# Kernel optimization log

Measured on AMD Instinct MI355X. Metric: run time of the kernel, lower is better.

## Reference

```python
import jax, jax.numpy as jnp
import numpy as np

DIM = 1024; VOCAB = 32000; HEADS = 16; HEAD_DIM = DIM // HEADS
SEG = 128; NPT = 16; WIDTH = 128
THETA = 0.1; ETA = 0.9; ALPHA = 0.01; EPS = 1e-6  # neural-memory lr / momentum / weight-decay


def l2n(x):
    return x / (jnp.linalg.norm(x, axis=-1, keepdims=True) + EPS)


def mlp(p, x):
    # 2-layer memory MLP: dim -> width -> dim, SiLU
    W1, b1, W2, b2 = p
    return jax.nn.silu(x @ W1 + b1) @ W2 + b2


def setup_inputs() -> dict:
    key = jax.random.key(0)
    ks = jax.random.split(key, 12)
    g = lambda k, s: jax.random.normal(k, s, jnp.float32) * 0.02
    z = lambda n: jnp.zeros((n,), jnp.float32)
    return {
        "x": jax.random.randint(ks[0], (2, 512), 0, VOCAB),
        "embedding": g(ks[1], (VOCAB, DIM)),
        "persistent": g(ks[2], (NPT, DIM)),
        "Wq": g(ks[3], (DIM, DIM)), "bq": z(DIM),
        "Wk": g(ks[4], (DIM, DIM)), "bk": z(DIM),
        "Wv": g(ks[5], (DIM, DIM)), "bv": z(DIM),
        "attn_in_w": g(ks[6], (DIM, 3 * DIM)), "attn_in_b": z(3 * DIM),
        "attn_out_w": g(ks[7], (DIM, DIM)), "attn_out_b": z(DIM),
        "mW1": g(ks[8], (DIM, WIDTH)), "mb1": z(WIDTH),
        "mW2": g(ks[9], (WIDTH, DIM)), "mb2": z(DIM),
        "head_w": g(ks[10], (DIM, VOCAB)), "head_b": z(VOCAB),
    }


def reference(x, embedding, persistent, Wq, bq, Wk, bk, Wv, bv,
              attn_in_w, attn_in_b, attn_out_w, attn_out_b,
              mW1, mb1, mW2, mb2, head_w, head_b):
    B, N = x.shape
    x_emb = embedding[x]  # [B, N, D]
    pad = (-N) % SEG
    if pad:
        x_emb = jnp.pad(x_emb, ((0, 0), (0, pad), (0, 0)))
    S = x_emb.shape[1] // SEG
    segs = x_emb.reshape(B, S, SEG, DIM).transpose(1, 0, 2, 3)  # [S, B, L, D]

    T = NPT + 2 * SEG  # persistent + retrieved memory + segment tokens
    causal = jnp.triu(jnp.ones((T, T), bool), 1)

    def mha(xc):  # [B, T, D] -> [B, T, D], torch nn.MultiheadAttention math
        q, k, v = jnp.split(xc @ attn_in_w + attn_in_b, 3, axis=-1)
        split = lambda t: t.reshape(B, T, HEADS, HEAD_DIM).transpose(0, 2, 1, 3)
        q, k, v = split(q), split(k), split(v)
        scores = jnp.einsum('bhqd,bhkd->bhqk', q, k) / np.sqrt(HEAD_DIM).astype(np.float32)
        scores = jnp.where(causal, -jnp.inf, scores)
        out = jnp.einsum('bhqk,bhkd->bhqd', jax.nn.softmax(scores, axis=-1), v)
        return out.transpose(0, 2, 1, 3).reshape(B, T, DIM) @ attn_out_w + attn_out_b

    # per-sample memory params (leading B axis) + zero momentum
    params0 = tuple(jnp.broadcast_to(w, (B,) + w.shape) for w in (mW1, mb1, mW2, mb2))
    mom0 = tuple(jnp.zeros_like(p) for p in params0)

    def mem_loss(p, k, v):
        e = mlp(p, k) - v
        return jnp.sum(e * e)

    def tok_step(carry, tok):  # tok: [B, D] -- one test-time gradient step on memory
        p, m = carry
        k = jax.lax.stop_gradient(l2n(tok @ Wk + bk))  # stop_grad_k=True
        v = tok @ Wv + bv                               # stop_grad_v=False
        grads = jax.vmap(jax.grad(mem_loss))(p, k, v)
        m = jax.tree.map(lambda mm, g: ETA * mm - THETA * g, m, grads)
        p = jax.tree.map(lambda pp, mm: (1.0 - ALPHA) * pp + mm, p, m)
        return (p, m), None

    retrieve = jax.vmap(mlp)  # vmap over per-sample memory params

    def seg_step(carry, segment):  # segment: [B, L, D]
        p, m = carry
        h = retrieve(p, l2n(segment @ Wq + bq))
        combined = jnp.concatenate(
            [jnp.broadcast_to(persistent, (B, NPT, DIM)), h, segment], axis=1)
        seg_out = mha(combined)[:, -SEG:, :]
        (p, m), _ = jax.lax.scan(tok_step, (p, m), seg_out.transpose(1, 0, 2))
        mem_out = retrieve(p, l2n(seg_out @ Wq + bq))
        return (p, m), seg_out * mem_out

    _, outs = jax.lax.scan(seg_step, (params0, mom0), segs)  # outs: [S, B, L, D]
    full = outs.transpose(1, 0, 2, 3).reshape(B, S * SEG, DIM)[:, :N, :]
    return full @ head_w + head_b
```

## Files before the change

kernel.cpp:

```cpp
#include <hip/hip_runtime.h>
#include <math.h>

#define D_    1024
#define B_    2
#define N_    512
#define SEG_  128
#define NSEG_ 4
#define NPT_  16
#define T_    272
#define NH_   16
#define HD_   64
#define W_    128
#define V_    32000

#define THETA_ 0.1f
#define ETA_   0.9f
#define PDEC_  0.99f
#define EPSN_  1e-6f
#define NBLK_ 16
#define FSTR_ 32

typedef __bf16 bf16x8 __attribute__((ext_vector_type(8)));
typedef float  f32x4  __attribute__((ext_vector_type(4)));

static const size_t XEMB = 0;
static const size_t OUTS = XEMB + (size_t)B_*N_*D_;
static const size_t PW1  = OUTS + (size_t)B_*N_*D_;
static const size_t PB1  = PW1  + (size_t)B_*D_*W_;
static const size_t PW2T = PB1  + (size_t)B_*W_;
static const size_t PB2  = PW2T + (size_t)B_*D_*W_;
static const size_t MOM  = PB2  + (size_t)B_*D_;
static const size_t MW1  = MOM;
static const size_t MB1  = MW1  + (size_t)B_*D_*W_;
static const size_t MW2T = MB1  + (size_t)B_*W_;
static const size_t MB2  = MW2T + (size_t)B_*D_*W_;
static const size_t MOMSZ = (size_t)B_*(D_*W_ + W_ + D_*W_ + D_);
static const size_t Q1   = MOM  + MOMSZ;
static const size_t AH   = Q1   + (size_t)B_*SEG_*D_;
static const size_t HBUF = AH   + (size_t)B_*SEG_*W_;
static const size_t COMB = HBUF + (size_t)B_*SEG_*D_;
static const size_t QKV  = COMB + (size_t)B_*T_*D_;
static const size_t ATTN = QKV  + (size_t)B_*T_*3*D_;
static const size_t SEGO = ATTN + (size_t)B_*SEG_*D_;
static const size_t KM   = SEGO + (size_t)B_*SEG_*D_;
static const size_t VM   = KM   + (size_t)B_*SEG_*D_;
static const size_t MEMO = VM   + (size_t)B_*SEG_*D_;
static const size_t WSEND = MEMO + (size_t)B_*SEG_*D_;

static const size_t AQ1K  = QKV;
static const size_t AQ1KM = AQ1K  + 32768;
static const size_t AGRAM = AQ1KM + 32768;
static const size_t ADZ1  = AGRAM + 32768;
static const size_t AA1H  = ADZ1  + 32768;
static const size_t AEH   = AA1H  + 32768;
static const size_t AEXA1 = AEH + (size_t)B_*SEG_*D_;
static const size_t AEXSP = AEXA1 + 512;
static const size_t AEXR  = AEXSP + 8192;
static const size_t AEXEE = AEXR  + 8192;
static const size_t COEF  = WSEND;
static const size_t ZEROB = COEF + 512;
static const size_t CBAR  = ZEROB + 128;

__device__ __forceinline__ float sigf(float x) { return 1.f/(1.f+expf(-x)); }

__device__ __forceinline__ void gstore(float* p, float v) {
  __hip_atomic_store(p, v, __ATOMIC_RELAXED, __HIP_MEMORY_SCOPE_AGENT);
}
__device__ __forceinline__ float gload(const float* p) {
  return __hip_atomic_load(p, __ATOMIC_RELAXED, __HIP_MEMORY_SCOPE_AGENT);
}

__device__ __forceinline__ void bsplit(float a, short& h, short& l) {
  unsigned u = __builtin_bit_cast(unsigned, a);
  unsigned hb = (u + 0x7fffu + ((u >> 16) & 1u)) >> 16;
  h = (short)hb;
  float hf = __builtin_bit_cast(float, hb << 16);
  float r = a - hf;
  unsigned ur = __builtin_bit_cast(unsigned, r);
  unsigned lb = (ur + 0x7fffu + ((ur >> 16) & 1u)) >> 16;
  l = (short)lb;
}

template<int BT, int SILU>
__global__ __launch_bounds__(256) void k_gemm(
    const float* __restrict__ A, const float* __restrict__ Bm,
    const float* __restrict__ bias, float* __restrict__ C,
    int M, int N, int K, long sA, long sB, long sC, long sBias)
{
  __shared__ float As[16][68];
  __shared__ float Bs[16][68];
  int bz = blockIdx.z;
  A += bz*sA; Bm += bz*sB; C += bz*sC; bias += bz*sBias;
  int n0 = blockIdx.x*64, m0 = blockIdx.y*64;
  int tid = threadIdx.x;
  int tx = tid & 15, ty = tid >> 4;
  int r  = tid >> 2;
  int kq = (tid & 3) * 4;
  float acc[4][4] = {};
  for (int k0 = 0; k0 < K; k0 += 16) {
    {
      int row = m0 + r;
      float4 v = make_float4(0.f,0.f,0.f,0.f);
      if (row < M) v = *(const float4*)(A + (long)row*K + k0 + kq);
      As[kq+0][r]=v.x; As[kq+1][r]=v.y; As[kq+2][r]=v.z; As[kq+3][r]=v.w;
    }
    if (BT) {
      int row = n0 + r;
      float4 v = *(const float4*)(Bm + (long)row*K + k0 + kq);
      Bs[kq+0][r]=v.x; Bs[kq+1][r]=v.y; Bs[kq+2][r]=v.z; Bs[kq+3][r]=v.w;
    } else {
      int c = tid & 63, r4 = tid >> 6;
      #pragma unroll
      for (int p = 0; p < 4; p++) {
        int kk = r4 + p*4;
        Bs[kk][c] = Bm[(long)(k0+kk)*N + n0 + c];
      }
    }
    __syncthreads();
    #pragma unroll
    for (int kk = 0; kk < 16; kk++) {
      float av[4], bv[4];
      #pragma unroll
      for (int i=0;i<4;i++) av[i] = As[kk][ty*4+i];
      #pragma unroll
      for (int j=0;j<4;j++) bv[j] = Bs[kk][tx*4+j];
      #pragma unroll
      for (int i=0;i<4;i++)
        #pragma unroll
        for (int j=0;j<4;j++)
          acc[i][j] = fmaf(av[i], bv[j], acc[i][j]);
    }
    __syncthreads();
  }
  #pragma unroll
  for (int i=0;i<4;i++) {
    int row = m0 + ty*4 + i;
    if (row >= M) continue;
    #pragma unroll
    for (int j=0;j<4;j++) {
      int col = n0 + tx*4 + j;
      float v = acc[i][j] + bias[col];
      if (SILU) v = v * sigf(v);
      C[(long)row*N + col] = v;
    }
  }
}

__global__ __launch_bounds__(256) void k_gemm2(
    const float* __restrict__ A, const float* __restrict__ B1,
    const float* __restrict__ B2, float* __restrict__ C1, float* __restrict__ C2,
    int K, long sA, long sB, long sC)
{
  __shared__ float As[16][68];
  __shared__ float B1s[16][68];
  __shared__ float B2s[16][68];
  int bz = blockIdx.z;
  A += bz*sA; B1 += bz*sB; B2 += bz*sB; C1 += bz*sC; C2 += bz*sC;
  int n0 = blockIdx.x*64, m0 = blockIdx.y*64;
  int tid = threadIdx.x;
  int tx = tid & 15, ty = tid >> 4;
  int r  = tid >> 2;
  int kq = (tid & 3) * 4;
  float acc1[4][4] = {}, acc2[4][4] = {};
  for (int k0 = 0; k0 < K; k0 += 16) {
    {
      float4 v = *(const float4*)(A + (long)(m0+r)*K + k0 + kq);
      As[kq+0][r]=v.x; As[kq+1][r]=v.y; As[kq+2][r]=v.z; As[kq+3][r]=v.w;
    }
    {
      int c = tid & 63, r4 = tid >> 6;
      #pragma unroll
      for (int p = 0; p < 4; p++) {
        int kk = r4 + p*4;
        B1s[kk][c] = B1[(long)(k0+kk)*W_ + n0 + c];
        B2s[kk][c] = B2[(long)(k0+kk)*W_ + n0 + c];
      }
    }
    __syncthreads();
    #pragma unroll
    for (int kk = 0; kk < 16; kk++) {
      float av[4], b1v[4], b2v[4];
      #pragma unroll
      for (int i=0;i<4;i++) av[i] = As[kk][ty*4+i];
      #pragma unroll
      for (int j=0;j<4;j++) { b1v[j] = B1s[kk][tx*4+j]; b2v[j] = B2s[kk][tx*4+j]; }
      #pragma unroll
      for (int i=0;i<4;i++)
        #pragma unroll
        for (int j=0;j<4;j++) {
          acc1[i][j] = fmaf(av[i], b1v[j], acc1[i][j]);
          acc2[i][j] = fmaf(av[i], b2v[j], acc2[i][j]);
        }
    }
    __syncthreads();
  }
  #pragma unroll
  for (int i=0;i<4;i++) {
    int row = m0 + ty*4 + i;
    #pragma unroll
    for (int j=0;j<4;j++) {
      int col = n0 + tx*4 + j;
      C1[(long)row*W_ + col] = acc1[i][j];
      C2[(long)row*W_ + col] = acc2[i][j];
    }
  }
}

__global__ __launch_bounds__(256) void k_gemm128(
    const float* __restrict__ A, const float* __restrict__ Bm,
    const float* __restrict__ bias, float* __restrict__ C,
    int M, int N, int K)
{
  __shared__ float As[16][132];
  __shared__ float Bs[16][132];
  int n0 = blockIdx.x*128, m0 = blockIdx.y*128;
  int tid = threadIdx.x;
  int tx = tid & 15, ty = tid >> 4;
  int ar = tid >> 1, ak = (tid & 1) * 8;
  int bk = tid >> 4, bn = (tid & 15) * 8;
  int arow = min(m0 + ar, M-1);
  float acc[8][8] = {};
  for (int k0 = 0; k0 < K; k0 += 16) {
    {
      const float* ap = A + (long)arow*K + k0 + ak;
      float4 v0 = *(const float4*)(ap);
      float4 v1 = *(const float4*)(ap+4);
      As[ak+0][ar]=v0.x; As[ak+1][ar]=v0.y; As[ak+2][ar]=v0.z; As[ak+3][ar]=v0.w;
      As[ak+4][ar]=v1.x; As[ak+5][ar]=v1.y; As[ak+6][ar]=v1.z; As[ak+7][ar]=v1.w;
      const float* bp = Bm + (long)(k0+bk)*N + n0 + bn;
      *(float4*)(&Bs[bk][bn])   = *(const float4*)(bp);
      *(float4*)(&Bs[bk][bn+4]) = *(const float4*)(bp+4);
    }
    __syncthreads();
    #pragma unroll
    for (int kk = 0; kk < 16; kk++) {
      float av[8], bv[8];
      #pragma unroll
      for (int i=0;i<8;i++) av[i] = As[kk][ty*8+i];
      #pragma unroll
      for (int j=0;j<8;j++) bv[j] = Bs[kk][tx*8+j];
      #pragma unroll
      for (int i=0;i<8;i++)
        #pragma unroll
        for (int j=0;j<8;j++)
          acc[i][j] = fmaf(av[i], bv[j], acc[i][j]);
    }
    __syncthreads();
  }
  #pragma unroll
  for (int i=0;i<8;i++) {
    int row = m0 + ty*8 + i;
    if (row >= M) continue;
    #pragma unroll
    for (int j=0;j<8;j++) acc[i][j] += bias[n0 + tx*8 + j];
    *(float4*)(C + (long)row*N + n0 + tx*8)     = make_float4(acc[i][0],acc[i][1],acc[i][2],acc[i][3]);
    *(float4*)(C + (long)row*N + n0 + tx*8 + 4) = make_float4(acc[i][4],acc[i][5],acc[i][6],acc[i][7]);
  }
}

__global__ __launch_bounds__(256) void k_head_mfma(
    const float* __restrict__ A, const float* __restrict__ Bm,
    const float* __restrict__ bias, float* __restrict__ C,
    int M, int N, int K)
{
  __shared__ short Ah[128][48];
  __shared__ short Al[128][48];
  __shared__ short Bh[32][132];
  __shared__ short Bl[32][132];
  int n0 = blockIdx.x*128, m0 = blockIdx.y*128;
  int tid = threadIdx.x;
  int wave = tid >> 6, lane = tid & 63;
  int wm = (wave >> 1) * 64, wn = (wave & 1) * 64;
  int lrow = lane & 15, lk = (lane >> 4) * 8;
  f32x4 acc[4][4] = {};
  for (int k0 = 0; k0 < K; k0 += 32) {
    __syncthreads();
    {
      int r = tid >> 1, kq = (tid & 1) * 16;
      const float* ap = A + (long)(m0 + r)*K + k0 + kq;
      #pragma unroll
      for (int q = 0; q < 16; q += 4) {
        float4 v = *(const float4*)(ap + q);
        short h0,l0,h1,l1,h2,l2,h3,l3;
        bsplit(v.x,h0,l0); bsplit(v.y,h1,l1); bsplit(v.z,h2,l2); bsplit(v.w,h3,l3);
        short4 hh = make_short4(h0,h1,h2,h3), ll = make_short4(l0,l1,l2,l3);
        *(short4*)&Ah[r][kq+q] = hh;
        *(short4*)&Al[r][kq+q] = ll;
      }
    }
    {
      int kr = tid >> 3, nq = (tid & 7) * 16;
      const float* bp = Bm + (long)(k0 + kr)*N + n0 + nq;
      #pragma unroll
      for (int q = 0; q < 16; q += 4) {
        float4 v = *(const float4*)(bp + q);
        short h0,l0,h1,l1,h2,l2,h3,l3;
        bsplit(v.x,h0,l0); bsplit(v.y,h1,l1); bsplit(v.z,h2,l2); bsplit(v.w,h3,l3);
        *(short4*)&Bh[kr][nq+q] = make_short4(h0,h1,h2,h3);
        *(short4*)&Bl[kr][nq+q] = make_short4(l0,l1,l2,l3);
      }
    }
    __syncthreads();
    bf16x8 bh[4], bl[4];
    #pragma unroll
    for (int nf = 0; nf < 4; nf++) {
      int col = wn + nf*16 + lrow;
      #pragma unroll
      for (int j = 0; j < 8; j++) {
        bh[nf][j] = __builtin_bit_cast(__bf16, Bh[lk+j][col]);
        bl[nf][j] = __builtin_bit_cast(__bf16, Bl[lk+j][col]);
      }
    }
    #pragma unroll
    for (int mf = 0; mf < 4; mf++) {
      int arow2 = wm + mf*16 + lrow;
      bf16x8 ah = *(const bf16x8*)&Ah[arow2][lk];
      bf16x8 al = *(const bf16x8*)&Al[arow2][lk];
      #pragma unroll
      for (int nf = 0; nf < 4; nf++) {
        acc[mf][nf] = __builtin_amdgcn_mfma_f32_16x16x32_bf16(ah, bh[nf], acc[mf][nf], 0, 0, 0);
        acc[mf][nf] = __builtin_amdgcn_mfma_f32_16x16x32_bf16(ah, bl[nf], acc[mf][nf], 0, 0, 0);
        acc[mf][nf] = __builtin_amdgcn_mfma_f32_16x16x32_bf16(al, bh[nf], acc[mf][nf], 0, 0, 0);
      }
    }
  }
  #pragma unroll
  for (int mf = 0; mf < 4; mf++) {
    #pragma unroll
    for (int nf = 0; nf < 4; nf++) {
      int col = n0 + wn + nf*16 + lrow;
      float bv = bias[col];
      #pragma unroll
      for (int j = 0; j < 4; j++) {
        int row = m0 + wm + mf*16 + (lane >> 4)*4 + j;
        C[(long)row*N + col] = acc[mf][nf][j] + bv;
      }
    }
  }
}

__global__ void k_embed(const int* __restrict__ x, const float* __restrict__ emb,
                        float* __restrict__ xe)
{
  int row = blockIdx.x, tid = threadIdx.x;
  int idx = x[row];
  float4 v = *(const float4*)(emb + (long)idx*D_ + tid*4);
  *(float4*)(xe + (long)row*D_ + tid*4) = v;
}

#define PER_ 263296L
__global__ void k_init(const float* __restrict__ mW1in, const float* __restrict__ mb1in,
                       const float* __restrict__ mW2in, const float* __restrict__ mb2in,
                       float* __restrict__ pW1, float* __restrict__ pb1,
                       float* __restrict__ pW2T, float* __restrict__ pb2)
{
  long g = (long)blockIdx.x*256 + threadIdx.x;
  if (g >= 2*PER_) return;
  int b = (int)(g / PER_);
  long rr = g % PER_;
  if (rr < 131072)       pW1[(long)b*131072 + rr] = mW1in[rr];
  else if (rr < 131200)  pb1[b*W_ + (rr-131072)] = mb1in[rr-131072];
  else if (rr < 262272) { long l = rr-131200; int j=(int)(l>>7), h=(int)(l&127);
                          pW2T[(long)b*131072 + l] = mW2in[(long)h*D_ + j]; }
  else                   pb2[b*D_ + (rr-262272)] = mb2in[rr-262272];
}

__global__ void k_coef(float* __restrict__ c)
{
  if (blockIdx.x == 0 && threadIdx.x == 0) {
    c[0] = 1.f; c[128] = 1.f;
    float A = 1.f, eta_d = 1.f;
    for (int d = 1; d < 128; d++) {
      eta_d *= ETA_;
      A = PDEC_*A + eta_d;
      c[d] = A;
      c[128 + d] = eta_d;
    }
    c[256] = 1.f;
    float bp = 1.f;
    for (int t = 1; t <= 128; t++) { bp *= PDEC_; c[256 + t] = bp; }
  }
}

__global__ __launch_bounds__(256) void k_l2n(float* __restrict__ X)
{
  long row = blockIdx.x;
  float* p = X + row*D_;
  int tid = threadIdx.x;
  float4 v = *(float4*)(p + tid*4);
  float ss = v.x*v.x + v.y*v.y + v.z*v.z + v.w*v.w;
  for (int o=32;o;o>>=1) ss += __shfl_xor(ss,o);
  __shared__ float wsum[4];
  if ((tid&63)==0) wsum[tid>>6] = ss;
  __syncthreads();
  float tot = wsum[0]+wsum[1]+wsum[2]+wsum[3];
  float sc = 1.f/(sqrtf(tot)+EPSN_);
  v.x*=sc; v.y*=sc; v.z*=sc; v.w*=sc;
  *(float4*)(p + tid*4) = v;
}

__global__ void k_concat(const float* __restrict__ pers, const float* __restrict__ h,
                         const float* __restrict__ xemb, int s, float* __restrict__ comb)
{
  int row = blockIdx.x, b = blockIdx.y, tid = threadIdx.x;
  const float* src;
  if (row < NPT_)            src = pers + (long)row*D_;
  else if (row < NPT_+SEG_)  src = h    + ((long)b*SEG_ + (row-NPT_))*D_;
  else                       src = xemb + ((long)b*N_ + s*SEG_ + (row-NPT_-SEG_))*D_;
  float4 v = *(const float4*)(src + tid*4);
  *(float4*)(comb + ((long)b*T_ + row)*D_ + tid*4) = v;
}

__global__ __launch_bounds__(256) void k_attn(const float* __restrict__ qkv,
                                              float* __restrict__ outp)
{
  __shared__ float sQ[16][68];
  __shared__ float sKV[64][68];
  __shared__ float sS[16][273];
  int qt = blockIdx.x, head = blockIdx.y, b = blockIdx.z;
  int tid = threadIdx.x;
  const float* base = qkv + (long)b*T_*3*D_;
  int qoff = head*HD_, koff = D_ + head*HD_, voff = 2*D_ + head*HD_;
  int qrow0 = NPT_ + SEG_ + qt*16;
  {
    int rr = tid>>4, c4 = (tid&15)*4;
    float4 v = *(const float4*)(base + (long)(qrow0+rr)*3*D_ + qoff + c4);
    sQ[rr][c4]=v.x; sQ[rr][c4+1]=v.y; sQ[rr][c4+2]=v.z; sQ[rr][c4+3]=v.w;
  }
  __syncthreads();
  for (int j0 = 0; j0 < T_; j0 += 64) {
    int chunk = min(64, T_ - j0);
    {
      int jj = tid>>2, cq = (tid&3)*16;
      if (jj < chunk) {
        #pragma unroll
        for (int q4=0;q4<4;q4++) {
          float4 v = *(const float4*)(base + (long)(j0+jj)*3*D_ + koff + cq + q4*4);
          sKV[jj][cq+q4*4]=v.x; sKV[jj][cq+q4*4+1]=v.y; sKV[jj][cq+q4*4+2]=v.z; sKV[jj][cq+q4*4+3]=v.w;
        }
      }
    }
    __syncthreads();
    int rr = tid>>4, jj0 = tid&15;
    #pragma unroll
    for (int p=0;p<4;p++) {
      int jj = jj0 + p*16;
      if (jj < chunk) {
        float s = 0.f;
        #pragma unroll 8
        for (int c=0;c<HD_;c++) s = fmaf(sQ[rr][c], sKV[jj][c], s);
        s *= 0.125f;
        int jg = j0 + jj, qg = qrow0 + rr;
        if (jg > qg) s = -3.0e38f;
        sS[rr][jg] = s;
      }
    }
    __syncthreads();
  }
  {
    int rr = tid>>4, l16 = tid&15;
    float m = -3.4e38f;
    for (int j=l16; j<T_; j+=16) m = fmaxf(m, sS[rr][j]);
    for (int o=8;o;o>>=1) m = fmaxf(m, __shfl_xor(m,o));
    float sum = 0.f;
    for (int j=l16; j<T_; j+=16) { float e = expf(sS[rr][j]-m); sS[rr][j] = e; sum += e; }
    for (int o=8;o;o>>=1) sum += __shfl_xor(sum,o);
    float inv = 1.f/sum;
    for (int j=l16; j<T_; j+=16) sS[rr][j] *= inv;
  }
  __syncthreads();
  float acc[4] = {0.f,0.f,0.f,0.f};
  int rr = tid>>4, c4 = (tid&15)*4;
  for (int j0 = 0; j0 < T_; j0 += 64) {
    int chunk = min(64, T_ - j0);
    {
      int jj = tid>>2, cq = (tid&3)*16;
      if (jj < chunk) {
        #pragma unroll
        for (int q4=0;q4<4;q4++) {
          float4 v = *(const float4*)(base + (long)(j0+jj)*3*D_ + voff + cq + q4*4);
          sKV[jj][cq+q4*4]=v.x; sKV[jj][cq+q4*4+1]=v.y; sKV[jj][cq+q4*4+2]=v.z; sKV[jj][cq+q4*4+3]=v.w;
        }
      }
    }
    __syncthreads();
    for (int jj=0; jj<chunk; jj++) {
      float p = sS[rr][j0+jj];
      #pragma unroll
      for (int i=0;i<4;i++) acc[i] = fmaf(p, sKV[jj][c4+i], acc[i]);
    }
    __syncthreads();
  }
  float4 o4 = make_float4(acc[0],acc[1],acc[2],acc[3]);
  *(float4*)(outp + ((long)(b*SEG_) + qt*16 + rr)*D_ + head*HD_ + c4) = o4;
}

__device__ __forceinline__ void gbar(int* flags, int blk, int gen)
{
  asm volatile("s_waitcnt vmcnt(0) lgkmcnt(0)" ::: "memory");
  __syncthreads();
  if (threadIdx.x == 0)
    __hip_atomic_store(flags + blk*FSTR_, gen, __ATOMIC_RELAXED, __HIP_MEMORY_SCOPE_AGENT);
  if (threadIdx.x < NBLK_) {
    while (__hip_atomic_load(flags + threadIdx.x*FSTR_, __ATOMIC_RELAXED,
                             __HIP_MEMORY_SCOPE_AGENT) < gen)
      __builtin_amdgcn_s_sleep(1);
  }
  __syncthreads();
}

__global__ __launch_bounds__(256) void k_scan(
  const float* __restrict__ pW2T, const float* __restrict__ mW2T,
  float* __restrict__ pb1, float* __restrict__ mb1,
  float* __restrict__ pb2, float* __restrict__ mb2,
  const float* __restrict__ Vm,
  const float* __restrict__ q1k, const float* __restrict__ q1km,
  const float* __restrict__ G,
  float* __restrict__ dz1o, float* __restrict__ a1o, float* __restrict__ eo,
  float* __restrict__ exA1, float* __restrict__ exSP,
  float* __restrict__ exR, float* __restrict__ exEE,
  const float* __restrict__ coef, int* __restrict__ barbase, int seg)
{
  __shared__ float sW[64][132];
  __shared__ float sMW[64][132];
  __shared__ float sEh[128][66];
  __shared__ float sA1h[128][9];
  __shared__ float sDZ[128][9];
  __shared__ float sQ1K[128][8];
  __shared__ float sQ1KM[128][8];
  __shared__ float sAt[128];
  __shared__ float sBp[129];
  __shared__ float sB1[8], sMB1[8], sZ1[8], sR[8];
  __shared__ float sB2[64], sMB2[64], sE[64];
  __shared__ float sA1t[128];
  __shared__ float sS[128];
  __shared__ float sEEc[128];

  int b = blockIdx.y, blk = blockIdx.x, tid = threadIdx.x;
  int j0 = blk*64, h0 = blk*8;
  int* flags = barbase + b*(NBLK_*FSTR_);
  int gbase = seg*1000;

  for (int i = tid; i < 64*128; i += 256) {
    int jj = i >> 7, h = i & 127;
    sW[jj][h]  = pW2T[(long)b*131072 + (long)(j0+jj)*128 + h];
    sMW[jj][h] = mW2T[(long)b*131072 + (long)(j0+jj)*128 + h];
  }
  for (int i = tid; i < 128*8; i += 256) {
    int t2 = i >> 3, hh = i & 7;
    sQ1K[t2][hh]  = q1k [((long)b*SEG_ + t2)*W_ + h0 + hh];
    sQ1KM[t2][hh] = q1km[((long)b*SEG_ + t2)*W_ + h0 + hh];
  }
  if (tid < 128) sAt[tid] = coef[tid];
  for (int i = tid; i < 129; i += 256) sBp[i] = coef[256 + i];
  if (tid < 8)  { sB1[tid] = pb1[b*W_ + h0 + tid]; sMB1[tid] = mb1[b*W_ + h0 + tid]; }
  if (tid >= 64 && tid < 128) {
    int jj = tid - 64;
    sB2[jj] = pb2[b*D_ + j0 + jj]; sMB2[jj] = mb2[b*D_ + j0 + jj];
  }
  __syncthreads();

  for (int t = 0; t < SEG_; ++t) {
    int par = t & 1;
    float bp = sBp[t];
    float ca = (t > 0) ? ETA_*sAt[t-1] : 0.f;

    if (t > 0 && tid < 8) {
      float mm = ETA_*sMB1[tid] - THETA_*sDZ[t-1][tid];
      sMB1[tid] = mm; sB1[tid] = PDEC_*sB1[tid] + mm;
    }
    __syncthreads();
    {
      int hh = tid >> 5, lane = tid & 31;
      float acc = 0.f;
      const float* Grow = G + ((long)b*SEG_ + t)*SEG_;
      for (int u = lane; u < t; u += 32)
        acc += sAt[t-1-u] * Grow[u] * sDZ[u][hh];
      for (int o = 16; o; o >>= 1) acc += __shfl_xor(acc, o);
      if (lane == 0) {
        int h = h0 + hh;
        float z1 = bp*sQ1K[t][hh] + ca*sQ1KM[t][hh] + sB1[hh] - THETA_*acc;
        sZ1[hh] = z1;
        float a1 = z1 * sigf(z1);
        sA1h[t][hh] = a1;
        gstore(&exA1[(long)par*(B_*W_) + b*W_ + h], a1);
      }
    }
    __syncthreads();
    if (tid < t) {
      float acc = 0.f;
      #pragma unroll
      for (int hh2 = 0; hh2 < 8; hh2++) acc += sA1h[tid][hh2]*sA1h[t][hh2];
      gstore(&exSP[(((long)par*B_ + b)*NBLK_ + blk)*W_ + tid], acc);
    }
    gbar(flags, blk, gbase + t*2 + 1);

    float rA1 = 0.f, rSP = 0.f;
    if (tid < 128) {
      rA1 = gload(&exA1[(long)par*(B_*W_) + b*W_ + tid]);
    } else {
      int u = tid - 128;
      if (u < t) {
        #pragma unroll
        for (int k2 = 0; k2 < NBLK_; k2++)
          rSP += gload(&exSP[(((long)par*B_ + b)*NBLK_ + k2)*W_ + u]);
      }
    }
    if (t > 0 && tid < 64) {
      float mm = ETA_*sMB2[tid] - 2.f*THETA_*sEh[t-1][tid];
      sMB2[tid] = mm; sB2[tid] = PDEC_*sB2[tid] + mm;
    }
    if (tid < 128) {
      sA1t[tid] = rA1;
    } else {
      int u = tid - 128;
      if (u < t) sS[u] = -2.f*THETA_*sAt[t-1-u]*rSP;
    }
    __syncthreads();
    {
      int jj = tid >> 2, l4 = tid & 3;
      float g0 = 0.f, gm = 0.f;
      for (int h = l4; h < 128; h += 4) {
        g0 = fmaf(sW[jj][h],  sA1t[h], g0);
        gm = fmaf(sMW[jj][h], sA1t[h], gm);
      }
      float corr = 0.f;
      for (int u = l4; u < t; u += 4) corr = fmaf(sS[u], sEh[u][jj], corr);
      float tot = bp*g0 + ca*gm + corr;
      tot += __shfl_xor(tot, 1); tot += __shfl_xor(tot, 2);
      if (l4 == 0) {
        float e = tot + sB2[jj] - Vm[((long)b*SEG_ + t)*D_ + j0 + jj];
        sEh[t][jj] = e; sE[jj] = e;
      }
    }
    __syncthreads();
    {
      int h = tid >> 1, l = tid & 1;
      float r0 = 0.f, rm = 0.f;
      for (int jj = l*32; jj < l*32+32; jj++) {
        r0 = fmaf(sW[jj][h],  sE[jj], r0);
        rm = fmaf(sMW[jj][h], sE[jj], rm);
      }
      float rc = bp*r0 + ca*rm;
      rc += __shfl_xor(rc, 1);
      if (l == 0) gstore(&exR[(((long)par*B_ + b)*NBLK_ + blk)*W_ + h], rc);
    }
    {
      int u = tid >> 1, l = tid & 1;
      if (u < t) {
        float acc = 0.f;
        for (int jj = l*32; jj < l*32+32; jj++) acc = fmaf(sEh[u][jj], sE[jj], acc);
        acc += __shfl_xor(acc, 1);
        if (l == 0) gstore(&exEE[(((long)par*B_ + b)*NBLK_ + blk)*W_ + u], acc);
      }
    }
    gbar(flags, blk, gbase + t*2 + 2);

    if (tid < t) {
      float s = 0.f;
      #pragma unroll
      for (int k2 = 0; k2 < NBLK_; k2++)
        s += gload(&exEE[(((long)par*B_ + b)*NBLK_ + k2)*W_ + tid]);
      sEEc[tid] = -2.f*THETA_*sAt[t-1-tid]*s;
    }
    if (tid >= 128 && tid < 136) {
      int hh = tid - 128;
      float s = 0.f;
      #pragma unroll
      for (int k2 = 0; k2 < NBLK_; k2++)
        s += gload(&exR[(((long)par*B_ + b)*NBLK_ + k2)*W_ + h0 + hh]);
      sR[hh] = s;
    }
    __syncthreads();
    {
      int hh = tid >> 5, lane = tid & 31;
      float acc = 0.f;
      for (int u = lane; u < t; u += 32) acc = fmaf(sEEc[u], sA1h[u][hh], acc);
      for (int o = 16; o; o >>= 1) acc += __shfl_xor(acc, o);
      if (lane == 0) {
        float z = sZ1[hh];
        float sg = sigf(z);
        float dz = 2.f*(sR[hh] + acc) * sg*(1.f + z*(1.f - sg));
        sDZ[t][hh] = dz;
      }
    }
    __syncthreads();
  }

  for (int i = tid; i < 128*8; i += 256) {
    int t2 = i >> 3, hh = i & 7;
    dz1o[((long)b*SEG_ + t2)*W_ + h0 + hh] = sDZ[t2][hh];
    a1o [((long)b*SEG_ + t2)*W_ + h0 + hh] = sA1h[t2][hh];
  }
  for (int i = tid; i < 128*64; i += 256) {
    int t2 = i >> 6, jj = i & 63;
    eo[((long)b*SEG_ + t2)*D_ + j0 + jj] = sEh[t2][jj];
  }
  if (tid < 8) {
    float mm = ETA_*sMB1[tid] - THETA_*sDZ[127][tid];
    mb1[b*W_ + h0 + tid] = mm;
    pb1[b*W_ + h0 + tid] = PDEC_*sB1[tid] + mm;
  } else if (tid >= 64 && tid < 128) {
    int jj = tid - 64;
    float mm = ETA_*sMB2[jj] - 2.f*THETA_*sEh[127][jj];
    mb2[b*D_ + j0 + jj] = mm;
    pb2[b*D_ + j0 + jj] = PDEC_*sB2[jj] + mm;
  }
}

__global__ __launch_bounds__(256) void k_recon(
  float* __restrict__ pW1, float* __restrict__ mW1,
  float* __restrict__ pW2T, float* __restrict__ mW2T,
  const float* __restrict__ KMp, const float* __restrict__ Eh,
  const float* __restrict__ DZ1, const float* __restrict__ A1h,
  const float* __restrict__ coef)
{
  __shared__ float s1[16][33];
  __shared__ float s2[16][65];
  __shared__ float sCA[128], sCE[128];
  int dt = blockIdx.x, ht = blockIdx.y, kb = blockIdx.z;
  int kind = kb >> 1, b = kb & 1;
  int tid = threadIdx.x;
  int d0 = dt*32, hb = ht*64;
  const float* in1 = (kind ? Eh : KMp) + (long)b*SEG_*D_;
  const float* in2 = (kind ? A1h : DZ1) + (long)b*SEG_*W_;
  float* Pb = (kind ? pW2T : pW1) + (long)b*131072;
  float* Mb = (kind ? mW2T : mW1) + (long)b*131072;
  float f = kind ? -2.f*THETA_ : -THETA_;
  if (tid < 128) {
    sCA[tid] = f*coef[127 - tid];
    sCE[tid] = f*coef[128 + 127 - tid];
  }
  __syncthreads();
  int dd = tid >> 3, le = tid & 7;
  float accP[8] = {}, accM[8] = {};
  for (int u0 = 0; u0 < 128; u0 += 16) {
    for (int i = tid; i < 16*32; i += 256) {
      int uu = i >> 5, d2 = i & 31;
      s1[uu][d2] = in1[(long)(u0+uu)*D_ + d0 + d2];
    }
    for (int i = tid; i < 16*64; i += 256) {
      int uu = i >> 6, hl = i & 63;
      s2[uu][hl] = in2[(long)(u0+uu)*W_ + hb + hl];
    }
    __syncthreads();
    #pragma unroll
    for (int uu = 0; uu < 16; uu++) {
      float a = s1[uu][dd];
      float cAu = sCA[u0+uu], cEu = sCE[u0+uu];
      #pragma unroll
      for (int k = 0; k < 8; k++) {
        float v = a * s2[uu][k*8 + le];
        accP[k] = fmaf(cAu, v, accP[k]);
        accM[k] = fmaf(cEu, v, accM[k]);
      }
    }
    __syncthreads();
  }
  float b128 = coef[256 + 128];
  float eA   = ETA_*coef[127];
  float e128 = ETA_*coef[128 + 127];
  #pragma unroll
  for (int k = 0; k < 8; k++) {
    long idx = (long)(d0+dd)*W_ + hb + k*8 + le;
    float Po = Pb[idx], Mo = Mb[idx];
    Pb[idx] = b128*Po + eA*Mo + accP[k];
    Mb[idx] = e128*Mo + accM[k];
  }
}

__global__ __launch_bounds__(256) void k_gemmkvq(
    const float* __restrict__ A,
    const float* __restrict__ Wk, const float* __restrict__ bk,
    const float* __restrict__ Wv, const float* __restrict__ bv,
    const float* __restrict__ Wq, const float* __restrict__ bq,
    float* __restrict__ KMo, float* __restrict__ VMo, float* __restrict__ Q1o)
{
  __shared__ float As[16][132];
  __shared__ float Bs[16][132];
  int bx = blockIdx.x;
  int sel = bx >> 3;
  int c0 = (bx & 7) * 128;
  int m0 = blockIdx.y * 128;
  const float* Bm   = sel == 0 ? Wk : sel == 1 ? Wv : Wq;
  const float* bias = sel == 0 ? bk : sel == 1 ? bv : bq;
  float* C          = sel == 0 ? KMo : sel == 1 ? VMo : Q1o;
  int tid = threadIdx.x;
  int tx = tid & 15, ty = tid >> 4;
  int ar = tid >> 1, ak = (tid & 1) * 8;
  int bkr = tid >> 4, bn = (tid & 15) * 8;
  float acc[8][8] = {};
  for (int k0 = 0; k0 < D_; k0 += 16) {
    {
      const float* ap = A + (long)(m0+ar)*D_ + k0 + ak;
      float4 v0 = *(const float4*)(ap);
      float4 v1 = *(const float4*)(ap+4);
      As[ak+0][ar]=v0.x; As[ak+1][ar]=v0.y; As[ak+2][ar]=v0.z; As[ak+3][ar]=v0.w;
      As[ak+4][ar]=v1.x; As[ak+5][ar]=v1.y; As[ak+6][ar]=v1.z; As[ak+7][ar]=v1.w;
      const float* bp = Bm + (long)(k0+bkr)*D_ + c0 + bn;
      *(float4*)(&Bs[bkr][bn])   = *(const float4*)(bp);
      *(float4*)(&Bs[bkr][bn+4]) = *(const float4*)(bp+4);
    }
    __syncthreads();
    #pragma unroll
    for (int kk = 0; kk < 16; kk++) {
      float av[8], bv8[8];
      #pragma unroll
      for (int i=0;i<8;i++) av[i] = As[kk][ty*8+i];
      #pragma unroll
      for (int j=0;j<8;j++) bv8[j] = Bs[kk][tx*8+j];
      #pragma unroll
      for (int i=0;i<8;i++)
        #pragma unroll
        for (int j=0;j<8;j++)
          acc[i][j] = fmaf(av[i], bv8[j], acc[i][j]);
    }
    __syncthreads();
  }
  #pragma unroll
  for (int i=0;i<8;i++) {
    int row = m0 + ty*8 + i;
    #pragma unroll
    for (int j=0;j<8;j++) acc[i][j] += bias[c0 + tx*8 + j];
    *(float4*)(C + (long)row*D_ + c0 + tx*8)     = make_float4(acc[i][0],acc[i][1],acc[i][2],acc[i][3]);
    *(float4*)(C + (long)row*D_ + c0 + tx*8 + 4) = make_float4(acc[i][4],acc[i][5],acc[i][6],acc[i][7]);
  }
}

__global__ void k_mul(const float* __restrict__ so, const float* __restrict__ mo,
                      float* __restrict__ outs, int s)
{
  int l = blockIdx.x, b = blockIdx.y, tid = threadIdx.x;
  long src = ((long)b*SEG_ + l)*D_ + tid*4;
  float4 a = *(const float4*)(so + src);
  float4 c = *(const float4*)(mo + src);
  a.x*=c.x; a.y*=c.y; a.z*=c.z; a.w*=c.w;
  *(float4*)(outs + ((long)b*N_ + s*SEG_ + l)*D_ + tid*4) = a;
}

static inline void gemm(const float* A, const float* Bm, const float* bias, float* C,
                        int M, int N, int K, long sA, long sB, long sC, long sBias,
                        int batch, int bt, int silu_, hipStream_t st)
{
  dim3 g(N/64, (M+63)/64, batch), blk(256);
  if (!bt && !silu_) k_gemm<0,0><<<g,blk,0,st>>>(A,Bm,bias,C,M,N,K,sA,sB,sC,sBias);
  else if (!bt && silu_) k_gemm<0,1><<<g,blk,0,st>>>(A,Bm,bias,C,M,N,K,sA,sB,sC,sBias);
  else k_gemm<1,0><<<g,blk,0,st>>>(A,Bm,bias,C,M,N,K,sA,sB,sC,sBias);
}

extern "C" void kernel_launch(void* const* d_in, const int* in_sizes, int n_in,
                              void* d_out, int out_size, void* d_ws, size_t ws_size,
                              hipStream_t stream)
{
  (void)in_sizes; (void)n_in; (void)out_size; (void)ws_size;
  const int*   x     = (const int*)  d_in[0];
  const float* emb   = (const float*)d_in[1];
  const float* pers  = (const float*)d_in[2];
  const float* Wq    = (const float*)d_in[3];
  const float* bq    = (const float*)d_in[4];
  const float* Wk    = (const float*)d_in[5];
  const float* bk    = (const float*)d_in[6];
  const float* Wv    = (const float*)d_in[7];
  const float* bv    = (const float*)d_in[8];
  const float* aiw   = (const float*)d_in[9];
  const float* aib   = (const float*)d_in[10];
  const float* aow   = (const float*)d_in[11];
  const float* aob   = (const float*)d_in[12];
  const float* mW1in = (const float*)d_in[13];
  const float* mb1in = (const float*)d_in[14];
  const float* mW2in = (const float*)d_in[15];
  const float* mb2in = (const float*)d_in[16];
  const float* headw = (const float*)d_in[17];
  const float* headb = (const float*)d_in[18];
  float* out = (float*)d_out;
  float* ws  = (float*)d_ws;

  hipMemsetAsync(ws + MOM, 0, MOMSZ*sizeof(float), stream);
  hipMemsetAsync(ws + ZEROB, 0, 128*sizeof(float), stream);
  hipMemsetAsync(ws + CBAR, 0, 1024*sizeof(int), stream);
  k_embed<<<dim3(B_*N_), dim3(256), 0, stream>>>(x, emb, ws+XEMB);
  k_init<<<dim3((2*PER_+255)/256), dim3(256), 0, stream>>>(
      mW1in, mb1in, mW2in, mb2in, ws+PW1, ws+PB1, ws+PW2T, ws+PB2);
  k_coef<<<dim3(1), dim3(64), 0, stream>>>(ws+COEF);

  for (int s = 0; s < NSEG_; s++) {
    const float* segA = ws + XEMB + (size_t)s*SEG_*D_;
    gemm(segA, Wq, bq, ws+Q1, SEG_, D_, D_, (long)N_*D_, 0, (long)SEG_*D_, 0, B_, 0, 0, stream);
    k_l2n<<<dim3(B_*SEG_), dim3(256), 0, stream>>>(ws+Q1);
    gemm(ws+Q1, ws+PW1, ws+PB1, ws+AH, SEG_, W_, D_, (long)SEG_*D_, (long)D_*W_, (long)SEG_*W_, W_, B_, 0, 1, stream);
    gemm(ws+AH, ws+PW2T, ws+PB2, ws+HBUF, SEG_, D_, W_, (long)SEG_*W_, (long)D_*W_, (long)SEG_*D_, D_, B_, 1, 0, stream);
    k_concat<<<dim3(T_, B_), dim3(256), 0, stream>>>(pers, ws+HBUF, ws+XEMB, s, ws+COMB);
    k_gemm128<<<dim3(3*D_/128, (B_*T_+127)/128), dim3(256), 0, stream>>>(
        ws+COMB, aiw, aib, ws+QKV, B_*T_, 3*D_, D_);
    k_attn<<<dim3(8, NH_, B_), dim3(256), 0, stream>>>(ws+QKV, ws+ATTN);
    gemm(ws+ATTN, aow, aob, ws+SEGO, B_*SEG_, D_, D_, 0, 0, 0, 0, 1, 0, 0, stream);
    k_gemmkvq<<<dim3(24, 2), dim3(256), 0, stream>>>(
        ws+SEGO, Wk, bk, Wv, bv, Wq, bq, ws+KM, ws+VM, ws+Q1);
    k_l2n<<<dim3(B_*SEG_), dim3(256), 0, stream>>>(ws+KM);
    k_l2n<<<dim3(B_*SEG_), dim3(256), 0, stream>>>(ws+Q1);
    k_gemm2<<<dim3(2, 2, B_), dim3(256), 0, stream>>>(
        ws+KM, ws+PW1, ws+MW1, ws+AQ1K, ws+AQ1KM,
        D_, (long)SEG_*D_, (long)D_*W_, (long)SEG_*W_);
    gemm(ws+KM, ws+KM,  ws+ZEROB, ws+AGRAM, SEG_, SEG_, D_, (long)SEG_*D_, (long)SEG_*D_, (long)SEG_*SEG_, 0, B_, 1, 0, stream);
    k_scan<<<dim3(NBLK_, B_), dim3(256), 0, stream>>>(
        ws+PW2T, ws+MW2T, ws+PB1, ws+MB1, ws+PB2, ws+MB2, ws+VM,
        ws+AQ1K, ws+AQ1KM, ws+AGRAM,
        ws+ADZ1, ws+AA1H, ws+AEH,
        ws+AEXA1, ws+AEXSP, ws+AEXR, ws+AEXEE,
        ws+COEF, (int*)(ws+CBAR), s);
    k_recon<<<dim3(32, 2, 4), dim3(256), 0, stream>>>(
        ws+PW1, ws+MW1, ws+PW2T, ws+MW2T,
        ws+KM, ws+AEH, ws+ADZ1, ws+AA1H, ws+COEF);
    gemm(ws+Q1, ws+PW1, ws+PB1, ws+AH, SEG_, W_, D_, (long)SEG_*D_, (long)D_*W_, (long)SEG_*W_, W_, B_, 0, 1, stream);
    gemm(ws+AH, ws+PW2T, ws+PB2, ws+MEMO, SEG_, D_, W_, (long)SEG_*W_, (long)D_*W_, (long)SEG_*D_, D_, B_, 1, 0, stream);
    k_mul<<<dim3(SEG_, B_), dim3(256), 0, stream>>>(ws+SEGO, ws+MEMO, ws+OUTS, s);
  }
  k_head_mfma<<<dim3(V_/128, (B_*N_)/128), dim3(256), 0, stream>>>(
      ws+OUTS, headw, headb, out, B_*N_, V_, D_);
}
```

Before: 8.681 ms.

## Restructure memory scan to one grid barrier per token with replicated hidden state

The sequential memory-update scan kernel now uses 32 blocks per batch instead of 16. Each block redundantly computes the full 128-wide hidden activations and their Gram products, which removes one of the two cross-block barriers per token. W2 rows are read from global memory each step instead of being staged in shared memory. This trades extra redundant compute and more global reads for half as many grid-wide synchronisations across the 128-step serial loop.

New measurement: 8.503 ms. 1.02x faster.

```diff
diff --git a/kernel.cpp b/kernel.cpp
--- a/kernel.cpp
+++ b/kernel.cpp
@@ -17,7 +17,7 @@
 #define ETA_   0.9f
 #define PDEC_  0.99f
 #define EPSN_  1e-6f
-#define NBLK_ 16
+#define NB2_  32
 #define FSTR_ 32
 
 typedef __bf16 bf16x8 __attribute__((ext_vector_type(8)));
@@ -53,10 +53,8 @@
 static const size_t ADZ1  = AGRAM + 32768;
 static const size_t AA1H  = ADZ1  + 32768;
 static const size_t AEH   = AA1H  + 32768;
-static const size_t AEXA1 = AEH + (size_t)B_*SEG_*D_;
-static const size_t AEXSP = AEXA1 + 512;
-static const size_t AEXR  = AEXSP + 8192;
-static const size_t AEXEE = AEXR  + 8192;
+static const size_t AEXR  = AEH + (size_t)B_*SEG_*D_;
+static const size_t AEXEE = AEXR + 16384;
 static const size_t COEF  = WSEND;
 static const size_t ZEROB = COEF + 512;
 static const size_t CBAR  = ZEROB + 128;
@@ -283,9 +281,8 @@
         float4 v = *(const float4*)(ap + q);
         short h0,l0,h1,l1,h2,l2,h3,l3;
         bsplit(v.x,h0,l0); bsplit(v.y,h1,l1); bsplit(v.z,h2,l2); bsplit(v.w,h3,l3);
-        short4 hh = make_short4(h0,h1,h2,h3), ll = make_short4(l0,l1,l2,l3);
-        *(short4*)&Ah[r][kq+q] = hh;
-        *(short4*)&Al[r][kq+q] = ll;
+        *(short4*)&Ah[r][kq+q] = make_short4(h0,h1,h2,h3);
+        *(short4*)&Al[r][kq+q] = make_short4(l0,l1,l2,l3);
       }
     }
     {
@@ -501,7 +498,7 @@
   __syncthreads();
   if (threadIdx.x == 0)
     __hip_atomic_store(flags + blk*FSTR_, gen, __ATOMIC_RELAXED, __HIP_MEMORY_SCOPE_AGENT);
-  if (threadIdx.x < NBLK_) {
+  if (threadIdx.x < NB2_) {
     while (__hip_atomic_load(flags + threadIdx.x*FSTR_, __ATOMIC_RELAXED,
                              __HIP_MEMORY_SCOPE_AGENT) < gen)
       __builtin_amdgcn_s_sleep(1);
@@ -517,194 +514,155 @@
   const float* __restrict__ q1k, const float* __restrict__ q1km,
   const float* __restrict__ G,
   float* __restrict__ dz1o, float* __restrict__ a1o, float* __restrict__ eo,
-  float* __restrict__ exA1, float* __restrict__ exSP,
   float* __restrict__ exR, float* __restrict__ exEE,
   const float* __restrict__ coef, int* __restrict__ barbase, int seg)
 {
-  __shared__ float sW[64][132];
-  __shared__ float sMW[64][132];
-  __shared__ float sEh[128][66];
-  __shared__ float sA1h[128][9];
-  __shared__ float sDZ[128][9];
-  __shared__ float sQ1K[128][8];
-  __shared__ float sQ1KM[128][8];
+  __shared__ float sDZ[128][129];
+  __shared__ float sA1[128][129];
+  __shared__ float sEh[128][33];
+  __shared__ float sB1[128], sMB1[128], sZ1[128], sR[128];
+  __shared__ float sB2[32], sMB2[32];
   __shared__ float sAt[128];
   __shared__ float sBp[129];
-  __shared__ float sB1[8], sMB1[8], sZ1[8], sR[8];
-  __shared__ float sB2[64], sMB2[64], sE[64];
-  __shared__ float sA1t[128];
+  __shared__ float sGc[128];
   __shared__ float sS[128];
   __shared__ float sEEc[128];
 
   int b = blockIdx.y, blk = blockIdx.x, tid = threadIdx.x;
-  int j0 = blk*64, h0 = blk*8;
-  int* flags = barbase + b*(NBLK_*FSTR_);
-  int gbase = seg*1000;
-
-  for (int i = tid; i < 64*128; i += 256) {
-    int jj = i >> 7, h = i & 127;
-    sW[jj][h]  = pW2T[(long)b*131072 + (long)(j0+jj)*128 + h];
-    sMW[jj][h] = mW2T[(long)b*131072 + (long)(j0+jj)*128 + h];
-  }
-  for (int i = tid; i < 128*8; i += 256) {
-    int t2 = i >> 3, hh = i & 7;
-    sQ1K[t2][hh]  = q1k [((long)b*SEG_ + t2)*W_ + h0 + hh];
-    sQ1KM[t2][hh] = q1km[((long)b*SEG_ + t2)*W_ + h0 + hh];
-  }
-  if (tid < 128) sAt[tid] = coef[tid];
-  for (int i = tid; i < 129; i += 256) sBp[i] = coef[256 + i];
-  if (tid < 8)  { sB1[tid] = pb1[b*W_ + h0 + tid]; sMB1[tid] = mb1[b*W_ + h0 + tid]; }
-  if (tid >= 64 && tid < 128) {
-    int jj = tid - 64;
-    sB2[jj] = pb2[b*D_ + j0 + jj]; sMB2[jj] = mb2[b*D_ + j0 + jj];
-  }
+  int j0 = blk*32;
+  int* flags = barbase + b*(NB2_*FSTR_);
+  int gbase = seg*200;
+  const float* W0 = pW2T + (long)b*131072;
+  const float* Wm = mW2T + (long)b*131072;
+
+  if (tid < 128) { sAt[tid] = coef[tid]; sB1[tid] = pb1[b*W_+tid]; sMB1[tid] = mb1[b*W_+tid]; }
+  else if (tid < 160) { int j = tid-128; sB2[j] = pb2[b*D_+j0+j]; sMB2[j] = mb2[b*D_+j0+j]; }
+  for (int i = tid; i < 129; i += 256) sBp[i] = coef[256+i];
   __syncthreads();
 
   for (int t = 0; t < SEG_; ++t) {
     int par = t & 1;
     float bp = sBp[t];
-    float ca = (t > 0) ? ETA_*sAt[t-1] : 0.f;
-
-    if (t > 0 && tid < 8) {
-      float mm = ETA_*sMB1[tid] - THETA_*sDZ[t-1][tid];
-      sMB1[tid] = mm; sB1[tid] = PDEC_*sB1[tid] + mm;
-    }
-    __syncthreads();
-    {
-      int hh = tid >> 5, lane = tid & 31;
+    float ca = (t>0) ? ETA_*sAt[t-1] : 0.f;
+
+    float rq1k = 0.f, rq1km = 0.f;
+    if (tid < 128) {
+      rq1k  = q1k [((long)b*SEG_+t)*W_ + tid];
+      rq1km = q1km[((long)b*SEG_+t)*W_ + tid];
+      if (t > 0) {
+        float mm = ETA_*sMB1[tid] - THETA_*sDZ[t-1][tid];
+        sMB1[tid] = mm; sB1[tid] = PDEC_*sB1[tid] + mm;
+      }
+      if (tid < t) sGc[tid] = sAt[t-1-tid]*G[((long)b*SEG_+t)*SEG_ + tid];
+    } else if (tid < 160) {
+      int j = tid-128;
+      if (t > 0) {
+        float mm = ETA_*sMB2[j] - 2.f*THETA_*sEh[t-1][j];
+        sMB2[j] = mm; sB2[j] = PDEC_*sB2[j] + mm;
+      }
+    }
+    __syncthreads();
+
+    if (tid < 128) {
       float acc = 0.f;
-      const float* Grow = G + ((long)b*SEG_ + t)*SEG_;
-      for (int u = lane; u < t; u += 32)
-        acc += sAt[t-1-u] * Grow[u] * sDZ[u][hh];
-      for (int o = 16; o; o >>= 1) acc += __shfl_xor(acc, o);
-      if (lane == 0) {
-        int h = h0 + hh;
-        float z1 = bp*sQ1K[t][hh] + ca*sQ1KM[t][hh] + sB1[hh] - THETA_*acc;
-        sZ1[hh] = z1;
-        float a1 = z1 * sigf(z1);
-        sA1h[t][hh] = a1;
-        gstore(&exA1[(long)par*(B_*W_) + b*W_ + h], a1);
-      }
-    }
-    __syncthreads();
+      for (int u = 0; u < t; ++u) acc = fmaf(sGc[u], sDZ[u][tid], acc);
+      float z1 = bp*rq1k + ca*rq1km + sB1[tid] - THETA_*acc;
+      sZ1[tid] = z1;
+      sA1[t][tid] = z1 * sigf(z1);
+    }
+    __syncthreads();
+
     if (tid < t) {
       float acc = 0.f;
-      #pragma unroll
-      for (int hh2 = 0; hh2 < 8; hh2++) acc += sA1h[tid][hh2]*sA1h[t][hh2];
-      gstore(&exSP[(((long)par*B_ + b)*NBLK_ + blk)*W_ + tid], acc);
-    }
-    gbar(flags, blk, gbase + t*2 + 1);
-
-    float rA1 = 0.f, rSP = 0.f;
+      #pragma unroll 8
+      for (int h = 0; h < 128; ++h) acc = fmaf(sA1[tid][h], sA1[t][h], acc);
+      sS[tid] = -2.f*THETA_*sAt[t-1-tid]*acc;
+    }
+    __syncthreads();
+
+    {
+      int j = tid >> 3, l = tid & 7;
+      const float* w0r = W0 + (long)(j0+j)*128;
+      const float* wmr = Wm + (long)(j0+j)*128;
+      float g = 0.f, gm = 0.f;
+      for (int h = l; h < 128; h += 8) {
+        g  = fmaf(w0r[h], sA1[t][h], g);
+        gm = fmaf(wmr[h], sA1[t][h], gm);
+      }
+      float corr = 0.f;
+      for (int u = l; u < t; u += 8) corr = fmaf(sS[u], sEh[u][j], corr);
+      float tot = bp*g + ca*gm + corr;
+      tot += __shfl_xor(tot,4); tot += __shfl_xor(tot,2); tot += __shfl_xor(tot,1);
+      if (l == 0) sEh[t][j] = tot + sB2[j] - Vm[((long)b*SEG_+t)*D_ + j0+j];
+    }
+    __syncthreads();
+
+    {
+      int h = tid >> 1, half = tid & 1;
+      float racc = 0.f;
+      for (int jj = half*16; jj < half*16+16; ++jj) {
+        float w = bp*W0[(long)(j0+jj)*128 + h] + ca*Wm[(long)(j0+jj)*128 + h];
+        racc = fmaf(w, sEh[t][jj], racc);
+      }
+      racc += __shfl_xor(racc,1);
+      if (half == 0) gstore(&exR[(((long)par*B_ + b)*NB2_ + blk)*W_ + h], racc);
+      if (h < t) {
+        float eacc = 0.f;
+        for (int jj = half*16; jj < half*16+16; ++jj)
+          eacc = fmaf(sEh[h][jj], sEh[t][jj], eacc);
+        eacc += __shfl_xor(eacc,1);
+        if (half == 0) gstore(&exEE[(((long)par*B_ + b)*NB2_ + blk)*W_ + h], eacc);
+      }
+    }
+    gbar(flags, blk, gbase + t + 1);
+
+    {
+      int h = tid >> 1, half = tid & 1;
+      float racc = 0.f;
+      #pragma unroll
+      for (int k = 0; k < 16; ++k)
+        racc += gload(&exR[(((long)par*B_ + b)*NB2_ + half*16 + k)*W_ + h]);
+      racc += __shfl_xor(racc,1);
+      if (half == 0) sR[h] = racc;
+      if (h < t) {
+        float eacc = 0.f;
+        #pragma unroll
+        for (int k = 0; k < 16; ++k)
+          eacc += gload(&exEE[(((long)par*B_ + b)*NB2_ + half*16 + k)*W_ + h]);
+        eacc += __shfl_xor(eacc,1);
+        if (half == 0) sEEc[h] = -2.f*THETA_*sAt[t-1-h]*eacc;
+      }
+    }
+    __syncthreads();
     if (tid < 128) {
-      rA1 = gload(&exA1[(long)par*(B_*W_) + b*W_ + tid]);
-    } else {
-      int u = tid - 128;
-      if (u < t) {
-        #pragma unroll
-        for (int k2 = 0; k2 < NBLK_; k2++)
-          rSP += gload(&exSP[(((long)par*B_ + b)*NBLK_ + k2)*W_ + u]);
-      }
-    }
-    if (t > 0 && tid < 64) {
-      float mm = ETA_*sMB2[tid] - 2.f*THETA_*sEh[t-1][tid];
-      sMB2[tid] = mm; sB2[tid] = PDEC_*sB2[tid] + mm;
-    }
-    if (tid < 128) {
-      sA1t[tid] = rA1;
-    } else {
-      int u = tid - 128;
-      if (u < t) sS[u] = -2.f*THETA_*sAt[t-1-u]*rSP;
-    }
-    __syncthreads();
-    {
-      int jj = tid >> 2, l4 = tid & 3;
-      float g0 = 0.f, gm = 0.f;
-      for (int h = l4; h < 128; h += 4) {
-        g0 = fmaf(sW[jj][h],  sA1t[h], g0);
-        gm = fmaf(sMW[jj][h], sA1t[h], gm);
-      }
-      float corr = 0.f;
-      for (int u = l4; u < t; u += 4) corr = fmaf(sS[u], sEh[u][jj], corr);
-      float tot = bp*g0 + ca*gm + corr;
-      tot += __shfl_xor(tot, 1); tot += __shfl_xor(tot, 2);
-      if (l4 == 0) {
-        float e = tot + sB2[jj] - Vm[((long)b*SEG_ + t)*D_ + j0 + jj];
-        sEh[t][jj] = e; sE[jj] = e;
-      }
-    }
-    __syncthreads();
-    {
-      int h = tid >> 1, l = tid & 1;
-      float r0 = 0.f, rm = 0.f;
-      for (int jj = l*32; jj < l*32+32; jj++) {
-        r0 = fmaf(sW[jj][h],  sE[jj], r0);
-        rm = fmaf(sMW[jj][h], sE[jj], rm);
-      }
-      float rc = bp*r0 + ca*rm;
-      rc += __shfl_xor(rc, 1);
-      if (l == 0) gstore(&exR[(((long)par*B_ + b)*NBLK_ + blk)*W_ + h], rc);
-    }
-    {
-      int u = tid >> 1, l = tid & 1;
-      if (u < t) {
-        float acc = 0.f;
-        for (int jj = l*32; jj < l*32+32; jj++) acc = fmaf(sEh[u][jj], sE[jj], acc);
-        acc += __shfl_xor(acc, 1);
-        if (l == 0) gstore(&exEE[(((long)par*B_ + b)*NBLK_ + blk)*W_ + u], acc);
-      }
-    }
-    gbar(flags, blk, gbase + t*2 + 2);
-
-    if (tid < t) {
-      float s = 0.f;
-      #pragma unroll
-      for (int k2 = 0; k2 < NBLK_; k2++)
-        s += gload(&exEE[(((long)par*B_ + b)*NBLK_ + k2)*W_ + tid]);
-      sEEc[tid] = -2.f*THETA_*sAt[t-1-tid]*s;
-    }
-    if (tid >= 128 && tid < 136) {
-      int hh = tid - 128;
-      float s = 0.f;
-      #pragma unroll
-      for (int k2 = 0; k2 < NBLK_; k2++)
-        s += gload(&exR[(((long)par*B_ + b)*NBLK_ + k2)*W_ + h0 + hh]);
-      sR[hh] = s;
-    }
-    __syncthreads();
-    {
-      int hh = tid >> 5, lane = tid & 31;
-      float acc = 0.f;
-      for (int u = lane; u < t; u += 32) acc = fmaf(sEEc[u], sA1h[u][hh], acc);
-      for (int o = 16; o; o >>= 1) acc += __shfl_xor(acc, o);
-      if (lane == 0) {
-        float z = sZ1[hh];
-        float sg = sigf(z);
-        float dz = 2.f*(sR[hh] + acc) * sg*(1.f + z*(1.f - sg));
-        sDZ[t][hh] = dz;
-      }
-    }
-    __syncthreads();
-  }
-
-  for (int i = tid; i < 128*8; i += 256) {
-    int t2 = i >> 3, hh = i & 7;
-    dz1o[((long)b*SEG_ + t2)*W_ + h0 + hh] = sDZ[t2][hh];
-    a1o [((long)b*SEG_ + t2)*W_ + h0 + hh] = sA1h[t2][hh];
-  }
-  for (int i = tid; i < 128*64; i += 256) {
-    int t2 = i >> 6, jj = i & 63;
-    eo[((long)b*SEG_ + t2)*D_ + j0 + jj] = sEh[t2][jj];
-  }
-  if (tid < 8) {
-    float mm = ETA_*sMB1[tid] - THETA_*sDZ[127][tid];
-    mb1[b*W_ + h0 + tid] = mm;
-    pb1[b*W_ + h0 + tid] = PDEC_*sB1[tid] + mm;
-  } else if (tid >= 64 && tid < 128) {
-    int jj = tid - 64;
-    float mm = ETA_*sMB2[jj] - 2.f*THETA_*sEh[127][jj];
-    mb2[b*D_ + j0 + jj] = mm;
-    pb2[b*D_ + j0 + jj] = PDEC_*sB2[jj] + mm;
+      float macc = 0.f;
+      for (int u = 0; u < t; ++u) macc = fmaf(sEEc[u], sA1[u][tid], macc);
+      float z = sZ1[tid], sg = sigf(z);
+      sDZ[t][tid] = 2.f*(sR[tid] + macc)*sg*(1.f + z*(1.f - sg));
+    }
+    __syncthreads();
+  }
+
+  if (tid < 128) {
+    if (blk == 0) {
+      float mm = ETA_*sMB1[tid] - THETA_*sDZ[127][tid];
+      mb1[b*W_ + tid] = mm;
+      pb1[b*W_ + tid] = PDEC_*sB1[tid] + mm;
+    }
+  } else if (tid < 160) {
+    int j = tid-128;
+    float mm = ETA_*sMB2[j] - 2.f*THETA_*sEh[127][j];
+    mb2[b*D_ + j0+j] = mm;
+    pb2[b*D_ + j0+j] = PDEC_*sB2[j] + mm;
+  }
+  for (int i = tid; i < 128*4; i += 256) {
+    int t2 = i >> 2, hh = (i & 3) + blk*4;
+    dz1o[((long)b*SEG_+t2)*W_ + hh] = sDZ[t2][hh];
+    a1o [((long)b*SEG_+t2)*W_ + hh] = sA1[t2][hh];
+  }
+  for (int i = tid; i < 128*32; i += 256) {
+    int t2 = i >> 5, jj = i & 31;
+    eo[((long)b*SEG_+t2)*D_ + j0+jj] = sEh[t2][jj];
   }
 }
 
@@ -877,7 +835,7 @@
 
   hipMemsetAsync(ws + MOM, 0, MOMSZ*sizeof(float), stream);
   hipMemsetAsync(ws + ZEROB, 0, 128*sizeof(float), stream);
-  hipMemsetAsync(ws + CBAR, 0, 1024*sizeof(int), stream);
+  hipMemsetAsync(ws + CBAR, 0, (size_t)B_*NB2_*FSTR_*sizeof(int), stream);
   k_embed<<<dim3(B_*N_), dim3(256), 0, stream>>>(x, emb, ws+XEMB);
   k_init<<<dim3((2*PER_+255)/256), dim3(256), 0, stream>>>(
       mW1in, mb1in, mW2in, mb2in, ws+PW1, ws+PB1, ws+PW2T, ws+PB2);
@@ -902,11 +860,11 @@
         ws+KM, ws+PW1, ws+MW1, ws+AQ1K, ws+AQ1KM,
         D_, (long)SEG_*D_, (long)D_*W_, (long)SEG_*W_);
     gemm(ws+KM, ws+KM,  ws+ZEROB, ws+AGRAM, SEG_, SEG_, D_, (long)SEG_*D_, (long)SEG_*D_, (long)SEG_*SEG_, 0, B_, 1, 0, stream);
-    k_scan<<<dim3(NBLK_, B_), dim3(256), 0, stream>>>(
+    k_scan<<<dim3(NB2_, B_), dim3(256), 0, stream>>>(
         ws+PW2T, ws+MW2T, ws+PB1, ws+MB1, ws+PB2, ws+MB2, ws+VM,
         ws+AQ1K, ws+AQ1KM, ws+AGRAM,
         ws+ADZ1, ws+AA1H, ws+AEH,
-        ws+AEXA1, ws+AEXSP, ws+AEXR, ws+AEXEE,
+        ws+AEXR, ws+AEXEE,
         ws+COEF, (int*)(ws+CBAR), s);
     k_recon<<<dim3(32, 2, 4), dim3(256), 0, stream>>>(
         ws+PW1, ws+MW1, ws+PW2T, ws+MW2T,
```
